# Kernel optimization log

Measured on AMD Instinct MI355X. Metric: run time of the kernel, lower is better.

The kernel has to match this reference:

```python
import jax, jax.numpy as jnp
import numpy as np

DIM = 1024
NUM_HEADS = 16
HEAD_DIM = DIM // NUM_HEADS


def setup_inputs() -> dict:
    key = jax.random.key(0)
    k1, k2, k3 = jax.random.split(key, 3)
    scale = 1.0 / np.sqrt(DIM)
    x = jax.random.normal(k1, (4, 2048, DIM), dtype=jnp.float32)
    w_qkv = jax.random.normal(k2, (DIM, 3 * DIM), dtype=jnp.float32) * scale
    b_qkv = jnp.zeros((3 * DIM,), dtype=jnp.float32)
    w_out = jax.random.normal(k3, (DIM, DIM), dtype=jnp.float32) * scale
    b_out = jnp.zeros((DIM,), dtype=jnp.float32)
    return {"x": x, "w_qkv": w_qkv, "b_qkv": b_qkv, "w_out": w_out, "b_out": b_out}


def reference(x, w_qkv, b_qkv, w_out, b_out):
    B, S, D = x.shape
    H, Hd = NUM_HEADS, HEAD_DIM
    qkv = x @ w_qkv + b_qkv  # [B,S,3D]
    q, k, v = jnp.split(qkv, 3, axis=-1)
    # [B,H,S,Hd]
    q = q.reshape(B, S, H, Hd).transpose(0, 2, 1, 3)
    k = k.reshape(B, S, H, Hd).transpose(0, 2, 1, 3)
    v = v.reshape(B, S, H, Hd).transpose(0, 2, 1, 3)
    scores = jnp.einsum('bhqd,bhkd->bhqk', q, k) / np.sqrt(Hd).astype(np.float32)
    causal = jnp.triu(jnp.ones((S, S), dtype=bool), k=1)  # True above diagonal -> masked
    scores = jnp.where(causal[None, None], -jnp.inf, scores)
    scores = scores - jnp.max(scores, axis=-1, keepdims=True)
    attn = jax.nn.softmax(scores, axis=-1)
    out = jnp.einsum('bhqk,bhkd->bhqd', attn, v)  # [B,H,S,Hd]
    out = out.transpose(0, 2, 1, 3).reshape(B, S, D)
    return out @ w_out + b_out
```

## Files before the change

### kernel.cpp

```cpp
#include <hip/hip_runtime.h>

typedef unsigned short u16;
typedef unsigned int u32;
using f32x4 = __attribute__((ext_vector_type(4))) float;
using f32x16 = __attribute__((ext_vector_type(16))) float;
using u32x4 = __attribute__((ext_vector_type(4))) u32;
typedef u32x4 __attribute__((may_alias)) u32x4a;
typedef uint2 __attribute__((may_alias)) uint2a;
using bf16x8 = __attribute__((ext_vector_type(8))) __bf16;

#define SEQ 2048

__device__ __forceinline__ u16 f2bf(float f) {
  union { float f; u32 u; } c; c.f = f;
  return (u16)((c.u + 0x7fffu + ((c.u >> 16) & 1u)) >> 16);
}
__device__ __forceinline__ float bf2f(u16 h) {
  union { u32 u; float f; } c; c.u = ((u32)h) << 16;
  return c.f;
}
__device__ __forceinline__ bf16x8 ld16(const u16* p) {
  return __builtin_bit_cast(bf16x8, *(const u32x4a*)p);
}
__device__ __forceinline__ f32x4 mfma16(bf16x8 a, bf16x8 b, f32x4 c) {
  return __builtin_amdgcn_mfma_f32_16x16x32_bf16(a, b, c, 0, 0, 0);
}
__device__ __forceinline__ f32x16 mfma32(bf16x8 a, bf16x8 b, f32x16 c) {
  return __builtin_amdgcn_mfma_f32_32x32x16_bf16(a, b, c, 0, 0, 0);
}
__device__ __forceinline__ void gload_lds16(const u16* g, u16* l) {
  __builtin_amdgcn_global_load_lds(
      (const __attribute__((address_space(1))) void*)g,
      (__attribute__((address_space(3))) void*)l, 16, 0, 0);
}
__device__ __forceinline__ u32 cvtpk(float lo, float hi) {
  u32 r;
  asm("v_cvt_pk_bf16_f32 %0, %1, %2" : "=v"(r) : "v"(lo), "v"(hi));
  return r;
}
__device__ __forceinline__ void plane32_swap(u32& a, u32& b) {
  asm("v_permlane32_swap_b32 %0, %1" : "+v"(a), "+v"(b));
}

__global__ void detect_dtype(const u16* __restrict__ x, int* __restrict__ flag) {
  if (threadIdx.x == 0) {
    int cnt = 0;
    for (int i = 0; i < 32; ++i) {
      const int e = (x[2 * i] >> 7) & 0xFF;
      cnt += (e >= 100 && e <= 140) ? 1 : 0;
    }
    *flag = (cnt >= 20) ? 1 : 0;
  }
}


__global__ __launch_bounds__(256)
void cvt_x(const void* __restrict__ in, u16* __restrict__ out,
           const int* __restrict__ flag, size_t eoff4) {
  const size_t i = (size_t)blockIdx.x * 256 + threadIdx.x;
  if (*flag) {
    ((uint2*)out)[i] = ((const uint2*)in)[eoff4 + i];
  } else {
    const float4 v = ((const float4*)in)[eoff4 + i];
    uint2 ov;
    ov.x = (u32)f2bf(v.x) | ((u32)f2bf(v.y) << 16);
    ov.y = (u32)f2bf(v.z) | ((u32)f2bf(v.w) << 16);
    ((uint2*)out)[i] = ov;
  }
}

__global__ __launch_bounds__(256)
void cvt_bias(const void* __restrict__ in, float* __restrict__ out, int n,
              const int* __restrict__ flag) {
  const int i = blockIdx.x * 256 + threadIdx.x;
  if (i >= n) return;
  out[i] = (*flag) ? bf2f(((const u16*)in)[i]) : ((const float*)in)[i];
}

__global__ __launch_bounds__(256)
void transpose_w(const void* __restrict__ in, u16* __restrict__ out, int K, int N,
                 const int* __restrict__ flag) {
  __shared__ float t[64][65];
  const int tid = threadIdx.x;
  const int r = tid >> 4, c4 = tid & 15;
  const int n0 = blockIdx.x << 6, k0 = blockIdx.y << 6;
  const int fl = *flag;
#pragma unroll
  for (int i = 0; i < 4; ++i) {
    const int kk = r + i * 16;
    const size_t base = (size_t)(k0 + kk) * N + n0 + c4 * 4;
    if (fl) {
      const uint2 raw = *(const uint2*)((const u16*)in + base);
      t[kk][c4 * 4 + 0] = bf2f((u16)(raw.x & 0xFFFF));
      t[kk][c4 * 4 + 1] = bf2f((u16)(raw.x >> 16));
      t[kk][c4 * 4 + 2] = bf2f((u16)(raw.y & 0xFFFF));
      t[kk][c4 * 4 + 3] = bf2f((u16)(raw.y >> 16));
    } else {
      const float4 v = *(const float4*)((const float*)in + base);
      t[kk][c4 * 4 + 0] = v.x; t[kk][c4 * 4 + 1] = v.y;
      t[kk][c4 * 4 + 2] = v.z; t[kk][c4 * 4 + 3] = v.w;
    }
  }
  __syncthreads();
#pragma unroll
  for (int i = 0; i < 4; ++i) {
    const int nn = r + i * 16;
    uint2 ov;
    ov.x = (u32)f2bf(t[c4 * 4 + 0][nn]) | ((u32)f2bf(t[c4 * 4 + 1][nn]) << 16);
    ov.y = (u32)f2bf(t[c4 * 4 + 2][nn]) | ((u32)f2bf(t[c4 * 4 + 3][nn]) << 16);
    *(uint2*)&out[(size_t)(n0 + nn) * K + k0 + c4 * 4] = ov;
  }
}

__global__ __launch_bounds__(256)
void transpose_v(const u16* __restrict__ qkv, u16* __restrict__ vt) {
  __shared__ __align__(16) u16 t[64][72];
  const int h = blockIdx.x, s0 = blockIdx.y << 6, b = blockIdx.z;
  const int tid = threadIdx.x;
  const int r = tid >> 2, g = tid & 3;
  const u16* src = &qkv[(size_t)(b * SEQ + s0 + r) * 3072 + 2048 + h * 64 + g * 16];
  *(u32x4a*)&t[r][g * 16]     = *(const u32x4a*)src;
  *(u32x4a*)&t[r][g * 16 + 8] = *(const u32x4a*)(src + 8);
  __syncthreads();
  union { u16 s[16]; u32x4 v[2]; } u;
#pragma unroll
  for (int e = 0; e < 16; ++e) u.s[e] = t[g * 16 + e][r];
  u16* dst = &vt[(size_t)((b * 16 + h) * 64 + r) * 2048 + s0 + g * 16];
  *(u32x4a*)dst = u.v[0];
  *(u32x4a*)(dst + 8) = u.v[1];
}

template <bool BF16_OUT>
__global__ __launch_bounds__(512, 2)
void gemm_bt(const u16* __restrict__ A, const u16* __restrict__ BT,
             const float* __restrict__ bias, void* __restrict__ Cv,
             int M, int N, int K) {
  constexpr int BK = 32;
  __shared__ __align__(16) u16 ring[4][12288];
  const int tid = threadIdx.x;
  const int wid = tid >> 6, lane = tid & 63;
  const int quad = lane >> 4, l16 = lane & 15;

  const int nbx = gridDim.x, nwg = nbx * gridDim.y;
  int bid = blockIdx.y * nbx + blockIdx.x;
  if ((nwg & 7) == 0) bid = (bid & 7) * (nwg >> 3) + (bid >> 3);
  const int tile_n = (bid % nbx) << 7;
  const int tile_m = (bid / nbx) << 8;

  const int wmR = (wid >> 1) << 6;
  const int wnR = (wid & 1) << 6;

  const int G0 = wid * 64 + lane;
  const int rA0 = G0 >> 2;
  const int sA0 = (((G0 & 3) ^ ((rA0 & 3) ^ ((rA0 >> 2) & 3)))) * 8;
  const int G1 = G0 + 512;
  const int rA1 = G1 >> 2;
  const int sA1 = (((G1 & 3) ^ ((rA1 & 3) ^ ((rA1 >> 2) & 3)))) * 8;
  const u16* const pA0 = A + (size_t)(tile_m + rA0) * K + sA0;
  const u16* const pA1 = A + (size_t)(tile_m + rA1) * K + sA1;
  const u16* const pB0 = BT + (size_t)(tile_n + rA0) * K + sA0;
  const int dst0 = wid * 512;
  const int dst1 = 4096 + wid * 512;
  const int dstB = 8192 + wid * 512;

  const int swl = (l16 & 3) ^ ((l16 >> 2) & 3);
  const int cA = (quad ^ swl) * 8;

  const int nk = K >> 5;
  f32x4 acc[4][4] = {};

  auto STAGE = [&](int kt) {
    u16* bp = ring[kt & 3];
    const size_t ko = (size_t)kt * BK;
    gload_lds16(pA0 + ko, bp + dst0);
    gload_lds16(pA1 + ko, bp + dst1);
    gload_lds16(pB0 + ko, bp + dstB);
  };

  STAGE(0);
  if (nk > 1) STAGE(1);
  if (nk > 2) STAGE(2);

  for (int kt = 0; kt < nk; ++kt) {
    asm volatile("s_waitcnt vmcnt(6)" ::: "memory");
    __builtin_amdgcn_sched_barrier(0);
    __builtin_amdgcn_s_barrier();
    __builtin_amdgcn_sched_barrier(0);
    if (kt + 3 < nk) STAGE(kt + 3);
    const u16* bp = ring[kt & 3];
    bf16x8 af[4], bfr[4];
#pragma unroll
    for (int i = 0; i < 4; ++i)
      af[i] = ld16(&bp[(wmR + i * 16 + l16) * BK + cA]);
#pragma unroll
    for (int j = 0; j < 4; ++j)
      bfr[j] = ld16(&bp[8192 + (wnR + j * 16 + l16) * BK + cA]);
    asm volatile("s_waitcnt lgkmcnt(0)" ::: "memory");
    __builtin_amdgcn_sched_barrier(0);
    __builtin_amdgcn_s_setprio(1);
#pragma unroll
    for (int i = 0; i < 4; ++i)
#pragma unroll
      for (int j = 0; j < 4; ++j) acc[i][j] = mfma16(af[i], bfr[j], acc[i][j]);
    __builtin_amdgcn_s_setprio(0);
  }

#pragma unroll
  for (int j = 0; j < 4; ++j) {
    const int cg = tile_n + wnR + j * 16 + l16;
    const float bv = bias[cg];
#pragma unroll
    for (int i = 0; i < 4; ++i) {
      const int rg = tile_m + wmR + i * 16 + quad * 4;
#pragma unroll
      for (int r = 0; r < 4; ++r) {
        const float v = acc[i][j][r] + bv;
        if constexpr (BF16_OUT)
          ((u16*)Cv)[(size_t)(rg + r) * N + cg] = f2bf(v);
        else
          ((float*)Cv)[(size_t)(rg + r) * N + cg] = v;
      }
    }
  }
}

__global__ __launch_bounds__(256, 2)
void attn_fwd(const u16* __restrict__ qkv, const u16* __restrict__ vt,
              u16* __restrict__ aout) {
  const int h = blockIdx.x, b = blockIdx.z;
  const int tid = threadIdx.x, wid = tid >> 6, lane = tid & 63;
  const int l31 = lane & 31, hi = lane >> 5;
  __shared__ __align__(16) u16 ring[4][8192];

  const int G0 = wid * 64 + lane, G1 = G0 + 256;
  const int r0 = G0 >> 3, c0 = ((G0 & 7) ^ (r0 & 7)) * 8;
  const int r1 = G1 >> 3, c1 = ((G1 & 7) ^ (r1 & 7)) * 8;
  const int db0 = wid * 512, db1 = 2048 + wid * 512;

  const u16* const kg = qkv + (size_t)(b * SEQ) * 3072 + 1024 + h * 64;
  const u16* const vg = vt + (size_t)((b * 16 + h) * 64) * 2048;

  constexpr float SC = 0.1803368801f;
  constexpr float THR = 44.3614196f;

  u32x4 onesu;
  onesu[0] = onesu[1] = onesu[2] = onesu[3] = 0x3F803F80u;
  const bf16x8 ones = __builtin_bit_cast(bf16x8, onesu);

  const int sx = l31 & 7;

  auto STAGE = [&](int kt) {
    u16* bp = ring[kt & 3];
    const int kb = kt * 64;
    gload_lds16(kg + (size_t)(kb + r0) * 3072 + c0, bp + db0);
    gload_lds16(kg + (size_t)(kb + r1) * 3072 + c1, bp + db1);
    gload_lds16(vg + (size_t)r0 * 2048 + kb + c0, bp + 4096 + db0);
    gload_lds16(vg + (size_t)r1 * 2048 + kb + c1, bp + 4096 + db1);
  };

#pragma unroll 1
  for (int pass = 0; pass < 2; ++pass) {
    const int qt = pass ? (int)blockIdx.y : 15 - (int)blockIdx.y;
    const int q0w = qt * 128 + wid * 32;
    const int qrow = q0w + l31;
    bf16x8 qf[4];
#pragma unroll
    for (int d = 0; d < 4; ++d)
      qf[d] = ld16(&qkv[(size_t)(b * SEQ + qrow) * 3072 + h * 64 + d * 16 + hi * 8]);
    f32x16 o0 = {}, o1 = {}, lacc = {};
    float m_r = -1e30f, ms = -1.8e29f;

    const int last = 2 * qt + 1;
    __syncthreads();
    STAGE(0);
    if (last >= 1) STAGE(1);
    if (last >= 2) STAGE(2);

#pragma unroll 1
    for (int kt = 0; kt <= last; ++kt) {
      const int rem = last - kt;
      if (rem >= 2)      asm volatile("s_waitcnt vmcnt(8)" ::: "memory");
      else if (rem == 1) asm volatile("s_waitcnt vmcnt(4)" ::: "memory");
      else               asm volatile("s_waitcnt vmcnt(0)" ::: "memory");
      __builtin_amdgcn_sched_barrier(0);
      __builtin_amdgcn_s_barrier();
      __builtin_amdgcn_sched_barrier(0);
      if (kt + 3 <= last) STAGE(kt + 3);
      const int kb = kt * 64;
      if (kb <= q0w + 31) {
        const u16* const lKc = ring[kt & 3];
        const u16* const lVc = ring[kt & 3] + 4096;
        f32x16 s0 = {}, s1 = {};
        bf16x8 kf0[4], kf1[4];
#pragma unroll
        for (int d = 0; d < 4; ++d) {
          kf0[d] = ld16(&lKc[l31 * 64 + (((d * 2 + hi) ^ sx)) * 8]);
          kf1[d] = ld16(&lKc[(32 + l31) * 64 + (((d * 2 + hi) ^ sx)) * 8]);
        }
        __builtin_amdgcn_s_setprio(1);
#pragma unroll
        for (int d = 0; d < 4; ++d) s0 = mfma32(kf0[d], qf[d], s0);
#pragma unroll
        for (int d = 0; d < 4; ++d) s1 = mfma32(kf1[d], qf[d], s1);
        __builtin_amdgcn_s_setprio(0);
        bf16x8 vf[2][2][2];
#pragma unroll
        for (int kh = 0; kh < 2; ++kh)
#pragma unroll
          for (int j = 0; j < 2; ++j)
#pragma unroll
            for (int dh = 0; dh < 2; ++dh)
              vf[kh][j][dh] = ld16(
                  &lVc[(dh * 32 + l31) * 64 + (((kh * 4 + j * 2 + hi) ^ sx)) * 8]);
        if (kb + 63 > q0w) {
          const int rel = qrow - kb - 4 * hi;
#pragma unroll
          for (int i = 0; i < 16; ++i) {
            const int kc = (i & 3) + 8 * (i >> 2);
            if (kc > rel) s0[i] = -1e30f;
            if (kc + 32 > rel) s1[i] = -1e30f;
          }
        }
        float pm = fmaxf(fmaxf(s0[0], s0[1]), s0[2]);
        pm = fmaxf(fmaxf(pm, s0[3]), s0[4]);
        pm = fmaxf(fmaxf(pm, s0[5]), s0[6]);
        pm = fmaxf(fmaxf(pm, s0[7]), s0[8]);
        pm = fmaxf(fmaxf(pm, s0[9]), s0[10]);
        pm = fmaxf(fmaxf(pm, s0[11]), s0[12]);
        pm = fmaxf(fmaxf(pm, s0[13]), s0[14]);
        pm = fmaxf(fmaxf(pm, s0[15]), s1[0]);
        pm = fmaxf(fmaxf(pm, s1[1]), s1[2]);
        pm = fmaxf(fmaxf(pm, s1[3]), s1[4]);
        pm = fmaxf(fmaxf(pm, s1[5]), s1[6]);
        pm = fmaxf(fmaxf(pm, s1[7]), s1[8]);
        pm = fmaxf(fmaxf(pm, s1[9]), s1[10]);
        pm = fmaxf(fmaxf(pm, s1[11]), s1[12]);
        pm = fmaxf(fmaxf(pm, s1[13]), s1[14]);
        pm = fmaxf(pm, s1[15]);
        if (__any(pm > m_r + THR)) {
          const float mm = fmaxf(pm, __shfl_xor(pm, 32));
          const float mn = fmaxf(m_r, mm);
          const float al = exp2f((m_r - mn) * SC);
#pragma unroll
          for (int i = 0; i < 16; ++i) {
            o0[i] *= al; o1[i] *= al; lacc[i] *= al;
          }
          m_r = mn;
          ms = mn * SC;
        }
#pragma unroll
        for (int i = 0; i < 16; ++i) {
          s0[i] = exp2f(fmaf(s0[i], SC, -ms));
          s1[i] = exp2f(fmaf(s1[i], SC, -ms));
        }
        u32 t0 = cvtpk(s0[0], s0[1]), t1 = cvtpk(s0[2], s0[3]);
        u32 t2 = cvtpk(s0[4], s0[5]), t3 = cvtpk(s0[6], s0[7]);
        u32 t4 = cvtpk(s0[8], s0[9]), t5 = cvtpk(s0[10], s0[11]);
        u32 t6 = cvtpk(s0[12], s0[13]), t7 = cvtpk(s0[14], s0[15]);
        plane32_swap(t0, t2); plane32_swap(t1, t3);
        plane32_swap(t4, t6); plane32_swap(t5, t7);
        u32x4 w00, w01;
        w00[0] = t0; w00[1] = t1; w00[2] = t2; w00[3] = t3;
        w01[0] = t4; w01[1] = t5; w01[2] = t6; w01[3] = t7;
        u32 u0 = cvtpk(s1[0], s1[1]), u1 = cvtpk(s1[2], s1[3]);
        u32 u2 = cvtpk(s1[4], s1[5]), u3 = cvtpk(s1[6], s1[7]);
        u32 u4 = cvtpk(s1[8], s1[9]), u5 = cvtpk(s1[10], s1[11]);
        u32 u6 = cvtpk(s1[12], s1[13]), u7 = cvtpk(s1[14], s1[15]);
        plane32_swap(u0, u2); plane32_swap(u1, u3);
        plane32_swap(u4, u6); plane32_swap(u5, u7);
        u32x4 w10, w11;
        w10[0] = u0; w10[1] = u1; w10[2] = u2; w10[3] = u3;
        w11[0] = u4; w11[1] = u5; w11[2] = u6; w11[3] = u7;
        const bf16x8 pb00 = __builtin_bit_cast(bf16x8, w00);
        const bf16x8 pb01 = __builtin_bit_cast(bf16x8, w01);
        const bf16x8 pb10 = __builtin_bit_cast(bf16x8, w10);
        const bf16x8 pb11 = __builtin_bit_cast(bf16x8, w11);
        __builtin_amdgcn_s_setprio(1);
        o0 = mfma32(vf[0][0][0], pb00, o0);
        o1 = mfma32(vf[0][0][1], pb00, o1);
        lacc = mfma32(ones, pb00, lacc);
        o0 = mfma32(vf[0][1][0], pb01, o0);
        o1 = mfma32(vf[0][1][1], pb01, o1);
        lacc = mfma32(ones, pb01, lacc);
        o0 = mfma32(vf[1][0][0], pb10, o0);
        o1 = mfma32(vf[1][0][1], pb10, o1);
        lacc = mfma32(ones, pb10, lacc);
        o0 = mfma32(vf[1][1][0], pb11, o0);
        o1 = mfma32(vf[1][1][1], pb11, o1);
        lacc = mfma32(ones, pb11, lacc);
        __builtin_amdgcn_s_setprio(0);
      }
    }
    const float inv = 1.0f / lacc[0];
    u16* const orow = &aout[(size_t)(b * SEQ + qrow) * 1024 + h * 64];
#pragma unroll
    for (int t = 0; t < 4; ++t) {
      const int d0 = 8 * t + 4 * hi;
      uint2a wv;
      wv.x = cvtpk(o0[4 * t] * inv, o0[4 * t + 1] * inv);
      wv.y = cvtpk(o0[4 * t + 2] * inv, o0[4 * t + 3] * inv);
      *(uint2a*)&orow[d0] = wv;
      wv.x = cvtpk(o1[4 * t] * inv, o1[4 * t + 1] * inv);
      wv.y = cvtpk(o1[4 * t + 2] * inv, o1[4 * t + 3] * inv);
      *(uint2a*)&orow[32 + d0] = wv;
    }
  }
}

extern "C" void kernel_launch(void* const* d_in, const int* in_sizes, int n_in,
                              void* d_out, int out_size, void* d_ws, size_t ws_size,
                              hipStream_t stream) {
  const void* x     = d_in[0];
  const void* w_qkv = d_in[1];
  const void* b_qkv = d_in[2];
  const void* w_out = d_in[3];
  const void* b_out = d_in[4];
  float* out = (float*)d_out;

  float* bqf   = (float*)d_ws;
  float* bof   = bqf + 3072;
  int*   flag  = (int*)(bof + 1024);
  u16*   wqkvT = (u16*)(flag + 4);
  u16*   woutT = wqkvT + (size_t)3072 * 1024;
  u16*   xb    = woutT + (size_t)1024 * 1024;

  detect_dtype<<<dim3(1), dim3(64), 0, stream>>>((const u16*)x, flag);
  cvt_bias<<<dim3(12), dim3(256), 0, stream>>>(b_qkv, bqf, 3072, flag);
  cvt_bias<<<dim3(4), dim3(256), 0, stream>>>(b_out, bof, 1024, flag);
  transpose_w<<<dim3(48, 16), dim3(256), 0, stream>>>(w_qkv, wqkvT, 1024, 3072, flag);
  transpose_w<<<dim3(16, 16), dim3(256), 0, stream>>>(w_out, woutT, 1024, 1024, flag);

  const size_t FULL_WS = 92291088;
  if (ws_size >= FULL_WS) {
    u16* qkv = xb  + (size_t)8192 * 1024;
    u16* vt  = qkv + (size_t)8192 * 3072;
    cvt_x<<<dim3(8192), dim3(256), 0, stream>>>(x, xb, flag, 0);
    gemm_bt<true ><<<dim3(24, 32), dim3(512), 0, stream>>>(xb, wqkvT, bqf, qkv,
                                                           8192, 3072, 1024);
    transpose_v<<<dim3(16, 32, 4), dim3(256), 0, stream>>>(qkv, vt);
    attn_fwd<<<dim3(16, 8, 4), dim3(256), 0, stream>>>(qkv, vt, xb);
    gemm_bt<false><<<dim3(8, 32), dim3(512), 0, stream>>>(xb, woutT, bof, out,
                                                          8192, 1024, 1024);
  } else {
    u16* qkvb = xb   + (size_t)2048 * 1024;
    u16* vtb  = qkvb + (size_t)2048 * 3072;
    for (int b = 0; b < 4; ++b) {
      const size_t eoff4 = (size_t)b * 2048 * 1024 / 4;
      cvt_x<<<dim3(2048), dim3(256), 0, stream>>>(x, xb, flag, eoff4);
      gemm_bt<true ><<<dim3(24, 8), dim3(512), 0, stream>>>(xb, wqkvT, bqf, qkvb,
                                                            2048, 3072, 1024);
      transpose_v<<<dim3(16, 32, 1), dim3(256), 0, stream>>>(qkvb, vtb);
      attn_fwd<<<dim3(16, 8, 1), dim3(256), 0, stream>>>(qkvb, vtb, xb);
      gemm_bt<false><<<dim3(8, 8), dim3(512), 0, stream>>>(
          xb, woutT, bof, out + (size_t)b * 2048 * 1024, 2048, 1024, 1024);
    }
  }
}
```

Before: 295.5 us.

## Enlarge GEMM tiles to 256x256 with split-phase A/B staging

```diff
diff --git a/kernel.cpp b/kernel.cpp
--- a/kernel.cpp
+++ b/kernel.cpp
@@ -136,65 +136,67 @@
              const float* __restrict__ bias, void* __restrict__ Cv,
              int M, int N, int K) {
   constexpr int BK = 32;
-  __shared__ __align__(16) u16 ring[4][12288];
+  __shared__ __align__(16) u16 ring[4][16384];
   const int tid = threadIdx.x;
   const int wid = tid >> 6, lane = tid & 63;
   const int quad = lane >> 4, l16 = lane & 15;
+  const int wm2 = wid >> 2, wn4 = wid & 3;
 
   const int nbx = gridDim.x, nwg = nbx * gridDim.y;
   int bid = blockIdx.y * nbx + blockIdx.x;
   if ((nwg & 7) == 0) bid = (bid & 7) * (nwg >> 3) + (bid >> 3);
-  const int tile_n = (bid % nbx) << 7;
+  const int tile_n = (bid % nbx) << 8;
   const int tile_m = (bid / nbx) << 8;
 
-  const int wmR = (wid >> 1) << 6;
-  const int wnR = (wid & 1) << 6;
-
-  const int G0 = wid * 64 + lane;
-  const int rA0 = G0 >> 2;
-  const int sA0 = (((G0 & 3) ^ ((rA0 & 3) ^ ((rA0 >> 2) & 3)))) * 8;
-  const int G1 = G0 + 512;
-  const int rA1 = G1 >> 2;
-  const int sA1 = (((G1 & 3) ^ ((rA1 & 3) ^ ((rA1 >> 2) & 3)))) * 8;
-  const u16* const pA0 = A + (size_t)(tile_m + rA0) * K + sA0;
-  const u16* const pA1 = A + (size_t)(tile_m + rA1) * K + sA1;
-  const u16* const pB0 = BT + (size_t)(tile_n + rA0) * K + sA0;
-  const int dst0 = wid * 512;
-  const int dst1 = 4096 + wid * 512;
-  const int dstB = 8192 + wid * 512;
-
-  const int swl = (l16 & 3) ^ ((l16 >> 2) & 3);
-  const int cA = (quad ^ swl) * 8;
+  const int r0 = tid >> 2, s0 = (tid & 3) ^ ((r0 >> 1) & 3);
+  const int G1 = tid + 512;
+  const int r1 = G1 >> 2, s1 = (G1 & 3) ^ ((r1 >> 1) & 3);
+  const u16* const pA0 = A + (size_t)(tile_m + r0) * K + s0 * 8;
+  const u16* const pA1 = A + (size_t)(tile_m + r1) * K + s1 * 8;
+  const u16* const pB0 = BT + (size_t)(tile_n + r0) * K + s0 * 8;
+  const u16* const pB1 = BT + (size_t)(tile_n + r1) * K + s1 * 8;
+  const int dw = wid * 512;
+
+  const int cA = (quad ^ ((l16 >> 1) & 3)) * 8;
+  const int aB = (wm2 * 128 + l16) * 32 + cA;
+  const int bB = 8192 + (wn4 * 64 + l16) * 32 + cA;
 
   const int nk = K >> 5;
-  f32x4 acc[4][4] = {};
-
-  auto STAGE = [&](int kt) {
-    u16* bp = ring[kt & 3];
-    const size_t ko = (size_t)kt * BK;
-    gload_lds16(pA0 + ko, bp + dst0);
-    gload_lds16(pA1 + ko, bp + dst1);
-    gload_lds16(pB0 + ko, bp + dstB);
+  f32x4 acc[8][4] = {};
+
+  auto STAGE_A = [&](int tt) {
+    u16* bp = &ring[tt & 3][0];
+    const size_t ko = (size_t)tt * BK;
+    gload_lds16(pA0 + ko, bp + dw);
+    gload_lds16(pA1 + ko, bp + 4096 + dw);
   };
-
-  STAGE(0);
-  if (nk > 1) STAGE(1);
-  if (nk > 2) STAGE(2);
-
-  for (int kt = 0; kt < nk; ++kt) {
-    asm volatile("s_waitcnt vmcnt(6)" ::: "memory");
+  auto STAGE_B = [&](int tt) {
+    u16* bp = &ring[tt & 3][8192];
+    const size_t ko = (size_t)tt * BK;
+    gload_lds16(pB0 + ko, bp + dw);
+    gload_lds16(pB1 + ko, bp + 4096 + dw);
+  };
+
+  STAGE_A(0); STAGE_B(0);
+  if (nk > 1) { STAGE_A(1); STAGE_B(1); }
+  if (nk > 2) { STAGE_A(2); STAGE_B(2); }
+
+#pragma unroll 1
+  for (int t = 0; t < nk; ++t) {
+    const int rem = nk - 1 - t;
+    if (rem >= 2)      asm volatile("s_waitcnt vmcnt(8)" ::: "memory");
+    else if (rem == 1) asm volatile("s_waitcnt vmcnt(4)" ::: "memory");
+    else               asm volatile("s_waitcnt vmcnt(0)" ::: "memory");
     __builtin_amdgcn_sched_barrier(0);
     __builtin_amdgcn_s_barrier();
     __builtin_amdgcn_sched_barrier(0);
-    if (kt + 3 < nk) STAGE(kt + 3);
-    const u16* bp = ring[kt & 3];
+    const u16* bp = ring[t & 3];
+    if (t + 3 < nk) STAGE_A(t + 3);
     bf16x8 af[4], bfr[4];
 #pragma unroll
-    for (int i = 0; i < 4; ++i)
-      af[i] = ld16(&bp[(wmR + i * 16 + l16) * BK + cA]);
-#pragma unroll
-    for (int j = 0; j < 4; ++j)
-      bfr[j] = ld16(&bp[8192 + (wnR + j * 16 + l16) * BK + cA]);
+    for (int i = 0; i < 4; ++i) af[i] = ld16(&bp[aB + i * 512]);
+#pragma unroll
+    for (int j = 0; j < 4; ++j) bfr[j] = ld16(&bp[bB + j * 512]);
     asm volatile("s_waitcnt lgkmcnt(0)" ::: "memory");
     __builtin_amdgcn_sched_barrier(0);
     __builtin_amdgcn_s_setprio(1);
@@ -203,15 +205,29 @@
 #pragma unroll
       for (int j = 0; j < 4; ++j) acc[i][j] = mfma16(af[i], bfr[j], acc[i][j]);
     __builtin_amdgcn_s_setprio(0);
+    __builtin_amdgcn_s_barrier();
+    __builtin_amdgcn_sched_barrier(0);
+    if (t + 3 < nk) STAGE_B(t + 3);
+#pragma unroll
+    for (int i = 0; i < 4; ++i) af[i] = ld16(&bp[aB + (i + 4) * 512]);
+    asm volatile("s_waitcnt lgkmcnt(0)" ::: "memory");
+    __builtin_amdgcn_sched_barrier(0);
+    __builtin_amdgcn_s_setprio(1);
+#pragma unroll
+    for (int i = 0; i < 4; ++i)
+#pragma unroll
+      for (int j = 0; j < 4; ++j)
+        acc[i + 4][j] = mfma16(af[i], bfr[j], acc[i + 4][j]);
+    __builtin_amdgcn_s_setprio(0);
   }
 
 #pragma unroll
   for (int j = 0; j < 4; ++j) {
-    const int cg = tile_n + wnR + j * 16 + l16;
+    const int cg = tile_n + wn4 * 64 + j * 16 + l16;
     const float bv = bias[cg];
 #pragma unroll
-    for (int i = 0; i < 4; ++i) {
-      const int rg = tile_m + wmR + i * 16 + quad * 4;
+    for (int i = 0; i < 8; ++i) {
+      const int rg = tile_m + wm2 * 128 + i * 16 + quad * 4;
 #pragma unroll
       for (int r = 0; r < 4; ++r) {
         const float v = acc[i][j][r] + bv;
@@ -435,11 +451,11 @@
     u16* qkv = xb  + (size_t)8192 * 1024;
     u16* vt  = qkv + (size_t)8192 * 3072;
     cvt_x<<<dim3(8192), dim3(256), 0, stream>>>(x, xb, flag, 0);
-    gemm_bt<true ><<<dim3(24, 32), dim3(512), 0, stream>>>(xb, wqkvT, bqf, qkv,
+    gemm_bt<true ><<<dim3(12, 32), dim3(512), 0, stream>>>(xb, wqkvT, bqf, qkv,
                                                            8192, 3072, 1024);
     transpose_v<<<dim3(16, 32, 4), dim3(256), 0, stream>>>(qkv, vt);
     attn_fwd<<<dim3(16, 8, 4), dim3(256), 0, stream>>>(qkv, vt, xb);
-    gemm_bt<false><<<dim3(8, 32), dim3(512), 0, stream>>>(xb, woutT, bof, out,
+    gemm_bt<false><<<dim3(4, 32), dim3(512), 0, stream>>>(xb, woutT, bof, out,
                                                           8192, 1024, 1024);
   } else {
     u16* qkvb = xb   + (size_t)2048 * 1024;
@@ -447,11 +463,11 @@
     for (int b = 0; b < 4; ++b) {
       const size_t eoff4 = (size_t)b * 2048 * 1024 / 4;
       cvt_x<<<dim3(2048), dim3(256), 0, stream>>>(x, xb, flag, eoff4);
-      gemm_bt<true ><<<dim3(24, 8), dim3(512), 0, stream>>>(xb, wqkvT, bqf, qkvb,
+      gemm_bt<true ><<<dim3(12, 8), dim3(512), 0, stream>>>(xb, wqkvT, bqf, qkvb,
                                                             2048, 3072, 1024);
       transpose_v<<<dim3(16, 32, 1), dim3(256), 0, stream>>>(qkvb, vtb);
       attn_fwd<<<dim3(16, 8, 1), dim3(256), 0, stream>>>(qkvb, vtb, xb);
-      gemm_bt<false><<<dim3(8, 8), dim3(512), 0, stream>>>(
+      gemm_bt<false><<<dim3(4, 8), dim3(512), 0, stream>>>(
           xb, woutT, bof, out + (size_t)b * 2048 * 1024, 2048, 1024, 1024);
     }
   }
```

After: 300.2 us. Within noise of the previous version (+1.6%).

## Shrink GEMM LDS ring to three stages and raise occupancy to four blocks

Applied to the files above, without the earlier changes.

```diff
diff --git a/kernel.cpp b/kernel.cpp
--- a/kernel.cpp
+++ b/kernel.cpp
@@ -131,12 +131,12 @@
 }
 
 template <bool BF16_OUT>
-__global__ __launch_bounds__(512, 2)
+__global__ __launch_bounds__(512, 4)
 void gemm_bt(const u16* __restrict__ A, const u16* __restrict__ BT,
              const float* __restrict__ bias, void* __restrict__ Cv,
              int M, int N, int K) {
   constexpr int BK = 32;
-  __shared__ __align__(16) u16 ring[4][12288];
+  __shared__ __align__(16) u16 ring[3][12288];
   const int tid = threadIdx.x;
   const int wid = tid >> 6, lane = tid & 63;
   const int quad = lane >> 4, l16 = lane & 15;
@@ -150,44 +150,42 @@
   const int wmR = (wid >> 1) << 6;
   const int wnR = (wid & 1) << 6;
 
-  const int G0 = wid * 64 + lane;
-  const int rA0 = G0 >> 2;
-  const int sA0 = (((G0 & 3) ^ ((rA0 & 3) ^ ((rA0 >> 2) & 3)))) * 8;
-  const int G1 = G0 + 512;
-  const int rA1 = G1 >> 2;
-  const int sA1 = (((G1 & 3) ^ ((rA1 & 3) ^ ((rA1 >> 2) & 3)))) * 8;
+  const int G0 = tid;
+  const int rA0 = G0 >> 2, sA0 = ((G0 & 3) ^ ((rA0 >> 1) & 3)) * 8;
+  const int G1 = tid + 512;
+  const int rA1 = G1 >> 2, sA1 = ((G1 & 3) ^ ((rA1 >> 1) & 3)) * 8;
   const u16* const pA0 = A + (size_t)(tile_m + rA0) * K + sA0;
   const u16* const pA1 = A + (size_t)(tile_m + rA1) * K + sA1;
   const u16* const pB0 = BT + (size_t)(tile_n + rA0) * K + sA0;
-  const int dst0 = wid * 512;
-  const int dst1 = 4096 + wid * 512;
-  const int dstB = 8192 + wid * 512;
-
-  const int swl = (l16 & 3) ^ ((l16 >> 2) & 3);
-  const int cA = (quad ^ swl) * 8;
+  const int dw = wid * 512;
+
+  const int cA = (quad ^ ((l16 >> 1) & 3)) * 8;
 
   const int nk = K >> 5;
   f32x4 acc[4][4] = {};
 
-  auto STAGE = [&](int kt) {
-    u16* bp = ring[kt & 3];
+  auto STAGE = [&](int kt, int buf) {
+    u16* bp = ring[buf];
     const size_t ko = (size_t)kt * BK;
-    gload_lds16(pA0 + ko, bp + dst0);
-    gload_lds16(pA1 + ko, bp + dst1);
-    gload_lds16(pB0 + ko, bp + dstB);
+    gload_lds16(pA0 + ko, bp + dw);
+    gload_lds16(pA1 + ko, bp + 4096 + dw);
+    gload_lds16(pB0 + ko, bp + 8192 + dw);
   };
 
-  STAGE(0);
-  if (nk > 1) STAGE(1);
-  if (nk > 2) STAGE(2);
-
-  for (int kt = 0; kt < nk; ++kt) {
-    asm volatile("s_waitcnt vmcnt(6)" ::: "memory");
+  STAGE(0, 0);
+  if (nk > 1) STAGE(1, 1);
+
+  int cur = 0;
+#pragma unroll 1
+  for (int t = 0; t < nk; ++t) {
+    if (t + 1 < nk) asm volatile("s_waitcnt vmcnt(3)" ::: "memory");
+    else            asm volatile("s_waitcnt vmcnt(0)" ::: "memory");
     __builtin_amdgcn_sched_barrier(0);
     __builtin_amdgcn_s_barrier();
     __builtin_amdgcn_sched_barrier(0);
-    if (kt + 3 < nk) STAGE(kt + 3);
-    const u16* bp = ring[kt & 3];
+    int sb = cur + 2; if (sb >= 3) sb -= 3;
+    if (t + 2 < nk) STAGE(t + 2, sb);
+    const u16* bp = ring[cur];
     bf16x8 af[4], bfr[4];
 #pragma unroll
     for (int i = 0; i < 4; ++i)
@@ -203,6 +201,7 @@
 #pragma unroll
       for (int j = 0; j < 4; ++j) acc[i][j] = mfma16(af[i], bfr[j], acc[i][j]);
     __builtin_amdgcn_s_setprio(0);
+    cur = (cur + 1 == 3) ? 0 : cur + 1;
   }
 
 #pragma unroll
```

Measured after the change: 286.8 us. 2.9% less time.
